# Performance work log

Hardware: AMD Instinct MI355X
Metric: run time of the kernel (lower is better)

Reference implementation:

```python
import jax, jax.numpy as jnp
import numpy as np

D_MODEL = 512
N_HEADS = 8
D_K = 64
B, T = 64, 256


def setup_inputs() -> dict:
    key = jax.random.key(0)
    ks = jax.random.split(key, 5)
    x = jax.random.normal(ks[0], (B, T, D_MODEL), dtype=jnp.float32)
    s = 1.0 / np.sqrt(D_MODEL)
    Wq = jax.random.normal(ks[1], (N_HEADS, D_MODEL, D_K), dtype=jnp.float32) * s
    Wk = jax.random.normal(ks[2], (N_HEADS, D_MODEL, D_K), dtype=jnp.float32) * s
    Wv = jax.random.normal(ks[3], (N_HEADS, D_MODEL, D_K), dtype=jnp.float32) * s
    Wo = jax.random.normal(ks[4], (N_HEADS * D_K, D_MODEL), dtype=jnp.float32) * s
    return {"x": x, "Wq": Wq, "Wk": Wk, "Wv": Wv, "Wo": Wo}


def reference(x, Wq, Wk, Wv, Wo):
    Bc, Tc, C = x.shape  # C == d_model; source scales by C**0.5, not sqrt(d_k)
    q = jnp.einsum('btc,hcd->bhtd', x, Wq)
    k = jnp.einsum('btc,hcd->bhtd', x, Wk)
    v = jnp.einsum('btc,hcd->bhtd', x, Wv)
    scores = jnp.einsum('bhtd,bhsd->bhts', q, k) / jnp.sqrt(jnp.float32(C))
    causal = jnp.tril(jnp.ones((Tc, Tc), dtype=bool))
    scores = jnp.where(causal, scores, -jnp.inf)
    attn = jax.nn.softmax(scores, axis=-1)  # dropout = identity in eval mode
    out = jnp.einsum('bhts,bhsd->bhtd', attn, v)
    out = out.transpose(0, 2, 1, 3).reshape(Bc, Tc, -1)  # concat heads
    return out @ Wo  # final dropout = identity in eval mode
```

## Files before the change

### kernel.cpp

```cpp
#include <hip/hip_runtime.h>
#include <hip/hip_bf16.h>

typedef __attribute__((ext_vector_type(4))) float f32x4;
typedef __attribute__((ext_vector_type(8))) short bf16x8;
typedef __attribute__((ext_vector_type(4))) short s16x4;
typedef __attribute__((ext_vector_type(4))) unsigned int u32x4;

#define DEV static __device__ __forceinline__

DEV unsigned short f2b(float f) {
  union { float f; unsigned int u; } v; v.f = f;
  unsigned int u = v.u;
  return (unsigned short)((u + 0x7fffu + ((u >> 16) & 1u)) >> 16);
}

DEV void gll16(const void* g, void* l) {
  __builtin_amdgcn_global_load_lds((__attribute__((address_space(1))) void*)g,
                                   (__attribute__((address_space(3))) void*)l,
                                   16, 0, 0);
}

__global__ __launch_bounds__(256) void prep(const float* __restrict__ x,
                                            const float* __restrict__ Wq,
                                            const float* __restrict__ Wk,
                                            const float* __restrict__ Wv,
                                            const float* __restrict__ Wo,
                                            unsigned short* __restrict__ xb,
                                            unsigned short* __restrict__ Wt,
                                            unsigned short* __restrict__ WoT) {
  const int bid = blockIdx.x;
  if (bid < 8192) {
    int id = bid * 256 + threadIdx.x;
    f32x4 v = *(const f32x4*)(x + (long)id * 4);
    s16x4 o;
    o.x = (short)f2b(v.x); o.y = (short)f2b(v.y);
    o.z = (short)f2b(v.z); o.w = (short)f2b(v.w);
    *(s16x4*)(xb + (long)id * 4) = o;
    return;
  }

  __shared__ unsigned int L[64 * 65];
  const int tx = threadIdx.x & 63;
  const int ty = threadIdx.x >> 6;

  int tb = bid - 8192;
  if (tb < 192) {
    int proj = tb >> 6, h = (tb >> 3) & 7, c0 = (tb & 7) << 6;
    const float* W = (proj == 0) ? Wq : ((proj == 1) ? Wk : Wv);
    const float* base = W + (long)h * 32768 + (long)c0 * 64;
#pragma unroll
    for (int i = 0; i < 16; i++) {
      int c = ty + i * 4;
      L[tx * 65 + c] = f2b(base[(long)c * 64 + tx]);
    }
    __syncthreads();
    unsigned short* out = Wt + ((long)(proj * 512 + h * 64)) * 512 + c0;
#pragma unroll
    for (int i = 0; i < 16; i++) {
      int d = ty + i * 4;
      out[(long)d * 512 + tx] = (unsigned short)L[d * 65 + tx];
    }
  } else {
    int t = tb - 192;
    int n0 = (t >> 3) << 6, c0 = (t & 7) << 6;
#pragma unroll
    for (int i = 0; i < 16; i++) {
      int c = ty + i * 4;
      L[tx * 65 + c] = f2b(Wo[(long)(c0 + c) * 512 + n0 + tx]);
    }
    __syncthreads();
    unsigned short* out = WoT + (long)n0 * 512 + c0;
#pragma unroll
    for (int i = 0; i < 16; i++) {
      int n = ty + i * 4;
      out[(long)n * 512 + tx] = (unsigned short)L[n * 65 + tx];
    }
  }
}

__global__ __launch_bounds__(512, 2) void qkv_attn(const unsigned short* __restrict__ xb,
                                                   const unsigned short* __restrict__ Wt,
                                                   unsigned short* __restrict__ AO) {
  __shared__ unsigned short SM[59904];
  const int QS_OFF = 0, KL_OFF = 16384, VT_OFF = 32768, PL_OFF = 49664;
  const int ASO[2] = {0, 16384};
  const int BSO[2] = {32768, 45056};

  const int tid = threadIdx.x;
  const int wave = tid >> 6, lane = tid & 63;
  const int quad = lane >> 4, l16 = lane & 15;

  const int xcd = blockIdx.x & 7, ci = blockIdx.x >> 3;
  const int wg = xcd * 64 + ci;
  const int b = wg >> 3, h = wg & 7;

  const unsigned short* Ag = xb + (long)b * 256 * 512;

  const int wm = wave >> 2, wn = wave & 3;
  const int srow = lane >> 3;
  const int scol = ((lane & 7) ^ srow) * 8;

  f32x4 acc[8][3] = {};

  auto stage = [&](int kk, int buf) {
#pragma unroll
    for (int s = 0; s < 4; s++) {
      int seg = wave * 4 + s;
      int row = seg * 8 + srow;
      gll16(Ag + (long)row * 512 + kk + scol, SM + ASO[buf] + seg * 512);
    }
#pragma unroll
    for (int s = 0; s < 3; s++) {
      int seg = wave * 3 + s;
      int proj = seg >> 3;
      int wrow = proj * 512 + h * 64 + (seg & 7) * 8 + srow;
      gll16(Wt + (long)wrow * 512 + kk + scol, SM + BSO[buf] + seg * 512);
    }
  };

  auto compute = [&](int buf) {
#pragma unroll
    for (int kc = 0; kc < 2; kc++) {
      const int rq = (((kc * 4 + quad) ^ (l16 & 7)) * 8);
      bf16x8 af[8], bfv[3];
#pragma unroll
      for (int mt = 0; mt < 8; mt++)
        af[mt] = *(const bf16x8*)(SM + ASO[buf] + (wm * 128 + mt * 16 + l16) * 64 + rq);
#pragma unroll
      for (int nt = 0; nt < 3; nt++)
        bfv[nt] = *(const bf16x8*)(SM + BSO[buf] + (wn * 48 + nt * 16 + l16) * 64 + rq);
#pragma unroll
      for (int mt = 0; mt < 8; mt++)
#pragma unroll
        for (int nt = 0; nt < 3; nt++)
          acc[mt][nt] = __builtin_amdgcn_mfma_f32_16x16x32_bf16(af[mt], bfv[nt], acc[mt][nt], 0, 0, 0);
    }
  };

  stage(0, 0);
  asm volatile("s_waitcnt vmcnt(0)" ::: "memory");
  __builtin_amdgcn_s_barrier();
  __builtin_amdgcn_sched_barrier(0);

  int cur = 0;
#pragma unroll
  for (int t = 0; t < 8; t++) {
    if (t < 7) stage((t + 1) * 64, cur ^ 1);
    __builtin_amdgcn_sched_barrier(0);
    compute(cur);
    if (t < 7) {
      asm volatile("s_waitcnt vmcnt(0)" ::: "memory");
      __builtin_amdgcn_s_barrier();
      __builtin_amdgcn_sched_barrier(0);
      cur ^= 1;
    }
  }

  __syncthreads();
#pragma unroll
  for (int mt = 0; mt < 8; mt++) {
#pragma unroll
    for (int nt = 0; nt < 3; nt++) {
      const int g = wn * 48 + nt * 16;
      const int proj = g >> 6;
      const int j0 = wm * 128 + mt * 16 + quad * 4;
      if (proj == 2) {
        int dcol = (g & 63) + l16;
        unsigned int w0 = (unsigned)f2b(acc[mt][nt][0]) | ((unsigned)f2b(acc[mt][nt][1]) << 16);
        unsigned int w1 = (unsigned)f2b(acc[mt][nt][2]) | ((unsigned)f2b(acc[mt][nt][3]) << 16);
        unsigned int* vp = (unsigned int*)(SM + VT_OFF + dcol * 264 + j0);
        vp[0] = w0; vp[1] = w1;
      } else {
        unsigned short* base = SM + (proj ? KL_OFF : QS_OFF);
        int d = (g & 63) + l16;
        int dhi = d >> 3, dlo = d & 7;
#pragma unroll
        for (int r2 = 0; r2 < 4; r2++) {
          int j = j0 + r2;
          base[j * 64 + ((dhi ^ (j & 7)) * 8) + dlo] = f2b(acc[mt][nt][r2]);
        }
      }
    }
  }
  __syncthreads();

  const int u = wave >> 1, par = wave & 1;
  const int tiles2[2] = {u, 7 - u};

  bf16x8 qf[2][2][2];
#pragma unroll
  for (int ti = 0; ti < 2; ti++)
#pragma unroll
    for (int kc = 0; kc < 2; kc++)
#pragma unroll
      for (int mt = 0; mt < 2; mt++) {
        int row = tiles2[ti] * 32 + mt * 16 + l16;
        qf[ti][kc][mt] = *(const bf16x8*)(SM + QS_OFF + row * 64 +
                                          (((kc * 4 + quad) ^ (row & 7)) * 8));
      }

  f32x4 O[2][2][4] = {};
  float lsum[2][2][4] = {};
  const float scale = 0.044194173824159216f;

#pragma unroll
  for (int ti = 0; ti < 2; ti++) {
    const int t = tiles2[ti];
    for (int c32 = par; c32 <= t; c32 += 2) {
      f32x4 S[2][2] = {};
#pragma unroll
      for (int kc = 0; kc < 2; kc++) {
        bf16x8 kbf[2];
#pragma unroll
        for (int st = 0; st < 2; st++) {
          int jrow = c32 * 32 + st * 16 + l16;
          kbf[st] = *(const bf16x8*)(SM + KL_OFF + jrow * 64 +
                                     (((kc * 4 + quad) ^ (jrow & 7)) * 8));
        }
#pragma unroll
        for (int mt = 0; mt < 2; mt++)
#pragma unroll
          for (int st = 0; st < 2; st++)
            S[mt][st] = __builtin_amdgcn_mfma_f32_16x16x32_bf16(qf[ti][kc][mt], kbf[st], S[mt][st], 0, 0, 0);
      }
      const bool diag = (c32 == t);
#pragma unroll
      for (int mt = 0; mt < 2; mt++)
#pragma unroll
        for (int st = 0; st < 2; st++)
#pragma unroll
          for (int r = 0; r < 4; r++) {
            int trow = mt * 16 + quad * 4 + r;
            float p = __expf(S[mt][st][r] * scale);
            if (diag && (st * 16 + l16 > trow)) p = 0.0f;
            lsum[ti][mt][r] += p;
            SM[PL_OFF + wave * 1280 + trow * 40 + st * 16 + l16] = f2b(p);
          }
      bf16x8 pa[2], vbf[4];
#pragma unroll
      for (int mt = 0; mt < 2; mt++)
        pa[mt] = *(const bf16x8*)(SM + PL_OFF + wave * 1280 + (mt * 16 + l16) * 40 + quad * 8);
#pragma unroll
      for (int dt = 0; dt < 4; dt++)
        vbf[dt] = *(const bf16x8*)(SM + VT_OFF + (dt * 16 + l16) * 264 + c32 * 32 + quad * 8);
#pragma unroll
      for (int mt = 0; mt < 2; mt++)
#pragma unroll
        for (int dt = 0; dt < 4; dt++)
          O[ti][mt][dt] = __builtin_amdgcn_mfma_f32_16x16x32_bf16(pa[mt], vbf[dt], O[ti][mt][dt], 0, 0, 0);
    }
  }

  float lred[2][2][4];
#pragma unroll
  for (int ti = 0; ti < 2; ti++)
#pragma unroll
    for (int mt = 0; mt < 2; mt++)
#pragma unroll
      for (int r = 0; r < 4; r++) {
        float s = lsum[ti][mt][r];
        s += __shfl_xor(s, 1); s += __shfl_xor(s, 2);
        s += __shfl_xor(s, 4); s += __shfl_xor(s, 8);
        lred[ti][mt][r] = s;
      }

  __syncthreads();

  float* Oscr = (float*)SM;
  float* Lscr = (float*)(SM + PL_OFF);

  if (par == 1) {
#pragma unroll
    for (int ti = 0; ti < 2; ti++)
#pragma unroll
      for (int mt = 0; mt < 2; mt++)
#pragma unroll
        for (int dt = 0; dt < 4; dt++)
#pragma unroll
          for (int r = 0; r < 4; r++)
            Oscr[u * 4096 + (ti * 32 + mt * 16 + quad * 4 + r) * 64 + dt * 16 + l16] = O[ti][mt][dt][r];
    if (l16 == 0)
#pragma unroll
      for (int ti = 0; ti < 2; ti++)
#pragma unroll
        for (int mt = 0; mt < 2; mt++)
#pragma unroll
          for (int r = 0; r < 4; r++)
            Lscr[u * 64 + ti * 32 + mt * 16 + quad * 4 + r] = lred[ti][mt][r];
  }
  __syncthreads();

  if (par == 0) {
    float linv[2][2][4];
#pragma unroll
    for (int ti = 0; ti < 2; ti++)
#pragma unroll
      for (int mt = 0; mt < 2; mt++)
#pragma unroll
        for (int r = 0; r < 4; r++)
          linv[ti][mt][r] = 1.0f / (lred[ti][mt][r] +
                                    Lscr[u * 64 + ti * 32 + mt * 16 + quad * 4 + r]);
#pragma unroll
    for (int ti = 0; ti < 2; ti++)
#pragma unroll
      for (int mt = 0; mt < 2; mt++)
#pragma unroll
        for (int dt = 0; dt < 4; dt++)
#pragma unroll
          for (int r = 0; r < 4; r++) {
            float o = O[ti][mt][dt][r] +
                      Oscr[u * 4096 + (ti * 32 + mt * 16 + quad * 4 + r) * 64 + dt * 16 + l16];
            int t_ = tiles2[ti] * 32 + mt * 16 + quad * 4 + r;
            int d = dt * 16 + l16;
            AO[(long)(b * 256 + t_) * 512 + h * 64 + d] = f2b(o * linv[ti][mt][r]);
          }
  }
}

template <int F32OUT>
__global__ __launch_bounds__(256, 2) void gemm_bt(const unsigned short* __restrict__ A,
                                                  const unsigned short* __restrict__ BT,
                                                  void* __restrict__ Cv,
                                                  int N) {
  const int K = 512;
  __shared__ unsigned short As[2][128 * 64];
  __shared__ unsigned short Bs[2][128 * 64];

  const int tid = threadIdx.x;
  const int wave = tid >> 6, lane = tid & 63;
  const int quad = lane >> 4, l16 = lane & 15;
  const int wm = wave >> 1, wn = wave & 1;

  const int NB = N >> 7;
  const int nwg = gridDim.x;
  const int q = nwg >> 3, r = nwg & 7;
  const int xcd = blockIdx.x & 7, ci = blockIdx.x >> 3;
  const int wg = (xcd < r ? xcd * (q + 1) : r * (q + 1) + (xcd - r) * q) + ci;
  const int bn = wg % NB;
  const int bm = wg / NB;

  const int srow = lane >> 3;
  const int scol = ((lane & 7) ^ srow) * 8;

  f32x4 acc[4][4] = {};

  auto stage = [&](int kk, int buf) {
#pragma unroll
    for (int s = 0; s < 4; s++) {
      int seg = wave * 4 + s;
      int row = seg * 8 + srow;
      gll16(A + (long)(bm * 128 + row) * K + kk + scol, &As[buf][seg * 512]);
      gll16(BT + (long)(bn * 128 + row) * K + kk + scol, &Bs[buf][seg * 512]);
    }
  };

  auto compute = [&](int buf) {
#pragma unroll
    for (int kc = 0; kc < 2; kc++) {
      const int rq = (((kc * 4 + quad) ^ (l16 & 7)) * 8);
      bf16x8 af[4], bfv[4];
#pragma unroll
      for (int mt = 0; mt < 4; mt++)
        af[mt] = *(const bf16x8*)(&As[buf][(wm * 64 + mt * 16 + l16) * 64 + rq]);
#pragma unroll
      for (int nt = 0; nt < 4; nt++)
        bfv[nt] = *(const bf16x8*)(&Bs[buf][(wn * 64 + nt * 16 + l16) * 64 + rq]);
#pragma unroll
      for (int mt = 0; mt < 4; mt++)
#pragma unroll
        for (int nt = 0; nt < 4; nt++)
          acc[mt][nt] = __builtin_amdgcn_mfma_f32_16x16x32_bf16(af[mt], bfv[nt], acc[mt][nt], 0, 0, 0);
    }
  };

  stage(0, 0);
  asm volatile("s_waitcnt vmcnt(0)" ::: "memory");
  __builtin_amdgcn_s_barrier();
  __builtin_amdgcn_sched_barrier(0);

  int cur = 0;
#pragma unroll
  for (int t = 0; t < 8; t++) {
    if (t < 7) stage((t + 1) * 64, cur ^ 1);
    __builtin_amdgcn_sched_barrier(0);
    compute(cur);
    if (t < 7) {
      asm volatile("s_waitcnt vmcnt(0)" ::: "memory");
      __builtin_amdgcn_s_barrier();
      __builtin_amdgcn_sched_barrier(0);
      cur ^= 1;
    }
  }

#pragma unroll
  for (int mt = 0; mt < 4; mt++) {
#pragma unroll
    for (int nt = 0; nt < 4; nt++) {
      int row0 = bm * 128 + wm * 64 + mt * 16 + quad * 4;
      int col = bn * 128 + wn * 64 + nt * 16 + l16;
      if (F32OUT) {
        float* cp = (float*)Cv + (long)row0 * N + col;
#pragma unroll
        for (int r2 = 0; r2 < 4; r2++)
          cp[(long)r2 * N] = acc[mt][nt][r2];
      } else {
        unsigned short* cp = (unsigned short*)Cv + (long)row0 * N + col;
#pragma unroll
        for (int r2 = 0; r2 < 4; r2++)
          cp[(long)r2 * N] = f2b(acc[mt][nt][r2]);
      }
    }
  }
}

extern "C" void kernel_launch(void* const* d_in, const int* in_sizes, int n_in,
                              void* d_out, int out_size, void* d_ws, size_t ws_size,
                              hipStream_t stream) {
  const float* x  = (const float*)d_in[0];
  const float* Wq = (const float*)d_in[1];
  const float* Wk = (const float*)d_in[2];
  const float* Wv = (const float*)d_in[3];
  const float* Wo = (const float*)d_in[4];

  unsigned short* Wt  = (unsigned short*)d_ws;
  unsigned short* WoT = Wt + 1536 * 512;
  unsigned short* xb  = WoT + 512 * 512;
  unsigned short* AO  = xb + (long)16384 * 512;
  float* out = (float*)d_out;

  prep<<<8448, 256, 0, stream>>>(x, Wq, Wk, Wv, Wo, xb, Wt, WoT);

  qkv_attn<<<512, 512, 0, stream>>>(xb, Wt, AO);

  gemm_bt<1><<<512, 256, 0, stream>>>(AO, WoT, (void*)out, 512);
}
```

Baseline: 148.2 us.

## Triple-buffer QKV projection with K=32 stages and partial waitcnt

Restructures the QKV projection mainloop from double-buffered K=64 steps to triple-buffered K=32 steps, with loads issued two stages ahead. A partial vmcnt wait replaces the full drain, so global-to-LDS copies for later stages stay in flight while the current stage computes. It also raises wave priority around the MFMA block. This adds more barriers per K and a new LDS swizzle for 32-wide rows, and the per-wave vmcnt counts must match the number of loads each wave issues.

After: 152.8 us. 1.03x slower.

```diff
diff --git a/kernel.cpp b/kernel.cpp
--- a/kernel.cpp
+++ b/kernel.cpp
@@ -83,8 +83,6 @@
                                                    unsigned short* __restrict__ AO) {
   __shared__ unsigned short SM[59904];
   const int QS_OFF = 0, KL_OFF = 16384, VT_OFF = 32768, PL_OFF = 49664;
-  const int ASO[2] = {0, 16384};
-  const int BSO[2] = {32768, 45056};
 
   const int tid = threadIdx.x;
   const int wave = tid >> 6, lane = tid & 63;
@@ -97,63 +95,69 @@
   const unsigned short* Ag = xb + (long)b * 256 * 512;
 
   const int wm = wave >> 2, wn = wave & 3;
-  const int srow = lane >> 3;
-  const int scol = ((lane & 7) ^ srow) * 8;
+  const int row16 = lane >> 2;
+  const int scg = ((lane & 3) ^ ((lane >> 3) & 3)) * 8;
 
   f32x4 acc[8][3] = {};
 
-  auto stage = [&](int kk, int buf) {
-#pragma unroll
-    for (int s = 0; s < 4; s++) {
-      int seg = wave * 4 + s;
-      int row = seg * 8 + srow;
-      gll16(Ag + (long)row * 512 + kk + scol, SM + ASO[buf] + seg * 512);
-    }
-#pragma unroll
-    for (int s = 0; s < 3; s++) {
-      int seg = wave * 3 + s;
-      int proj = seg >> 3;
-      int wrow = proj * 512 + h * 64 + (seg & 7) * 8 + srow;
-      gll16(Wt + (long)wrow * 512 + kk + scol, SM + BSO[buf] + seg * 512);
+  auto stageP1 = [&](int t, int buf) {
+    unsigned short* base = SM + buf * 14336;
+#pragma unroll
+    for (int i = 0; i < 2; i++) {
+      int sa = wave * 2 + i;
+      gll16(Ag + (long)(sa * 16 + row16) * 512 + t * 32 + scg, base + sa * 512);
+    }
+    {
+      int sb = wave;
+      int brow = sb * 16 + row16;
+      int wrow = (sb >> 2) * 512 + h * 64 + (brow & 63);
+      gll16(Wt + (long)wrow * 512 + t * 32 + scg, base + 8192 + sb * 512);
+    }
+    if (wave < 4) {
+      int sb = 8 + wave;
+      int brow = sb * 16 + row16;
+      int wrow = (sb >> 2) * 512 + h * 64 + (brow & 63);
+      gll16(Wt + (long)wrow * 512 + t * 32 + scg, base + 8192 + sb * 512);
     }
   };
 
-  auto compute = [&](int buf) {
-#pragma unroll
-    for (int kc = 0; kc < 2; kc++) {
-      const int rq = (((kc * 4 + quad) ^ (l16 & 7)) * 8);
-      bf16x8 af[8], bfv[3];
-#pragma unroll
-      for (int mt = 0; mt < 8; mt++)
-        af[mt] = *(const bf16x8*)(SM + ASO[buf] + (wm * 128 + mt * 16 + l16) * 64 + rq);
+  const int rq32 = (quad ^ ((l16 >> 1) & 3)) * 8;
+
+  auto computeP1 = [&](int buf) {
+    const unsigned short* base = SM + buf * 14336;
+    bf16x8 af[8], bfv[3];
+#pragma unroll
+    for (int mt = 0; mt < 8; mt++)
+      af[mt] = *(const bf16x8*)(base + (wm * 128 + mt * 16 + l16) * 32 + rq32);
+#pragma unroll
+    for (int nt = 0; nt < 3; nt++)
+      bfv[nt] = *(const bf16x8*)(base + 8192 + (wn * 48 + nt * 16 + l16) * 32 + rq32);
+#pragma unroll
+    for (int mt = 0; mt < 8; mt++)
 #pragma unroll
       for (int nt = 0; nt < 3; nt++)
-        bfv[nt] = *(const bf16x8*)(SM + BSO[buf] + (wn * 48 + nt * 16 + l16) * 64 + rq);
-#pragma unroll
-      for (int mt = 0; mt < 8; mt++)
-#pragma unroll
-        for (int nt = 0; nt < 3; nt++)
-          acc[mt][nt] = __builtin_amdgcn_mfma_f32_16x16x32_bf16(af[mt], bfv[nt], acc[mt][nt], 0, 0, 0);
-    }
+        acc[mt][nt] = __builtin_amdgcn_mfma_f32_16x16x32_bf16(af[mt], bfv[nt], acc[mt][nt], 0, 0, 0);
   };
 
-  stage(0, 0);
-  asm volatile("s_waitcnt vmcnt(0)" ::: "memory");
-  __builtin_amdgcn_s_barrier();
-  __builtin_amdgcn_sched_barrier(0);
-
-  int cur = 0;
-#pragma unroll
-  for (int t = 0; t < 8; t++) {
-    if (t < 7) stage((t + 1) * 64, cur ^ 1);
+  stageP1(0, 0);
+  stageP1(1, 1);
+
+#pragma unroll
+  for (int t = 0; t < 16; t++) {
+    if (t < 15) {
+      if (wave < 4) asm volatile("s_waitcnt vmcnt(4)" ::: "memory");
+      else          asm volatile("s_waitcnt vmcnt(3)" ::: "memory");
+    } else {
+      asm volatile("s_waitcnt vmcnt(0)" ::: "memory");
+    }
+    __builtin_amdgcn_s_barrier();
     __builtin_amdgcn_sched_barrier(0);
-    compute(cur);
-    if (t < 7) {
-      asm volatile("s_waitcnt vmcnt(0)" ::: "memory");
-      __builtin_amdgcn_s_barrier();
-      __builtin_amdgcn_sched_barrier(0);
-      cur ^= 1;
-    }
+    if (t < 14) stageP1(t + 2, (t + 2) % 3);
+    __builtin_amdgcn_sched_barrier(0);
+    __builtin_amdgcn_s_setprio(1);
+    computeP1(t % 3);
+    __builtin_amdgcn_s_setprio(0);
+    __builtin_amdgcn_sched_barrier(0);
   }
 
   __syncthreads();
```
